# Kernel tuning notes

Measured on AMD Instinct MI355X. Metric: run time of the kernel, lower is better.

The kernel has to match this reference:

```python
import jax, jax.numpy as jnp
import numpy as np

WINDOW = 60
DEPTH = 3
HIDDEN = 256
LN_EPS = 1e-5


def _lyndon_indices(d):
    # Lyndon words over alphabet {0..d-1}, lengths 2 and 3, lexicographic order
    # (signatory mode='words' extracts expanded-logsig coefficients at Lyndon words).
    i2 = np.array([(i, j) for i in range(d) for j in range(d) if (i, j) < (j, i)], dtype=np.int32)
    i3 = np.array([(i, j, k) for i in range(d) for j in range(d) for k in range(d)
                   if (i, j, k) < (j, k, i) and (i, j, k) < (k, i, j)], dtype=np.int32)
    return i2, i3


def _logsig_features(x):
    # x: [b, s, c] -> logsignature of time-augmented sliding windows: [b*s, sig_channels]
    b, s, c = x.shape
    d = c + 1
    # replicate-padded sliding windows via clipped gather (matches F.pad replicate + unfold)
    pos = jnp.clip(jnp.arange(s)[:, None] + jnp.arange(WINDOW)[None, :] - (WINDOW - 1), 0, s - 1)
    windows = x[:, pos, :]                                   # [b, s, W, c]
    t = jnp.linspace(0.0, 1.0, WINDOW, dtype=x.dtype)        # time augmentation channel
    t_b = jnp.broadcast_to(t[None, None, :, None], (b, s, WINDOW, 1))
    aug = jnp.concatenate([t_b, windows], axis=-1).reshape(b * s, WINDOW, d)
    N = b * s
    # basepoint=True: prepend zero point -> increments include the first point itself
    inc = jnp.diff(aug, axis=1, prepend=jnp.zeros((N, 1, d), aug.dtype))  # [N, W, d]
    inc_t = jnp.transpose(inc, (1, 0, 2))                    # [W, N, d]

    def chen_step(carry, v):
        S1, S2, S3 = carry
        vv = jnp.einsum('ni,nj->nij', v, v)
        vvv = jnp.einsum('nij,nk->nijk', vv, v)
        nS3 = S3 + jnp.einsum('nij,nk->nijk', S2, v) \
                 + 0.5 * jnp.einsum('ni,njk->nijk', S1, vv) + vvv / 6.0
        nS2 = S2 + jnp.einsum('ni,nj->nij', S1, v) + 0.5 * vv
        nS1 = S1 + v
        return (nS1, nS2, nS3), None

    init = (jnp.zeros((N, d), x.dtype), jnp.zeros((N, d, d), x.dtype), jnp.zeros((N, d, d, d), x.dtype))
    (S1, S2, S3), _ = jax.lax.scan(chen_step, init, inc_t)
    # log in truncated tensor algebra: log(1+x) = x - x^2/2 + x^3/3
    L1 = S1
    L2 = S2 - 0.5 * jnp.einsum('ni,nj->nij', S1, S1)
    L3 = (S3 - 0.5 * (jnp.einsum('ni,njk->nijk', S1, S2) + jnp.einsum('nij,nk->nijk', S2, S1))
          + jnp.einsum('ni,nj,nk->nijk', S1, S1, S1) / 3.0)
    i2, i3 = _lyndon_indices(d)
    f2 = L2[:, i2[:, 0], i2[:, 1]]
    f3 = L3[:, i3[:, 0], i3[:, 1], i3[:, 2]]
    return jnp.concatenate([L1, f2, f3], axis=-1)            # [N, sig_channels]


def setup_inputs() -> dict:
    key = jax.random.key(0)
    ks = jax.random.split(key, 5)
    b, s, c = 8, 2048, 8
    d = c + 1
    sig_channels = d + (d * d - d) // 2 + (d ** 3 - d) // 3  # 285 for d=9
    h2 = 2 * HIDDEN
    x = jax.random.normal(ks[0], (b, s, c), dtype=jnp.float32)
    w1 = jax.random.normal(ks[1], (sig_channels, h2), dtype=jnp.float32) / np.sqrt(sig_channels)
    b1 = jnp.zeros((h2,), jnp.float32)
    ln_g = jnp.ones((h2,), jnp.float32)
    ln_b = jnp.zeros((h2,), jnp.float32)
    w2 = jax.random.normal(ks[2], (h2, HIDDEN), dtype=jnp.float32) / np.sqrt(h2)
    b2 = jnp.zeros((HIDDEN,), jnp.float32)
    return {"x": x, "w1": w1, "b1": b1, "ln_g": ln_g, "ln_b": ln_b, "w2": w2, "b2": b2}


def reference(x, w1, b1, ln_g, ln_b, w2, b2):
    b, s, _ = x.shape
    feats = _logsig_features(x)                              # [b*s, sig_channels]
    h = jax.nn.gelu(feats @ w1 + b1, approximate=False)      # torch default GELU (erf)
    mu = jnp.mean(h, axis=-1, keepdims=True)
    var = jnp.var(h, axis=-1, keepdims=True)
    h = (h - mu) / jnp.sqrt(var + LN_EPS) * ln_g + ln_b      # LayerNorm; Dropout is eval no-op
    out = h @ w2 + b2
    return out.reshape(b, s, -1)
```

## Files before the change

kernel.cpp:

```cpp
#include <hip/hip_runtime.h>
#include <hip/hip_bf16.h>
#include <cstdint>
#include <cstddef>

typedef short short8 __attribute__((ext_vector_type(8)));
typedef float f32x4 __attribute__((ext_vector_type(4)));
typedef float f32x2 __attribute__((ext_vector_type(2)));

#define NS    2048
#define KPAD  288
#define H2    512
#define HID   256
#define WPB   7
#define SBLK  293

#define MFMA(a,b,c) __builtin_amdgcn_mfma_f32_16x16x32_bf16((a),(b),(c),0,0,0)

__device__ __forceinline__ void gl2lds16(const void* g, void* l) {
    __builtin_amdgcn_global_load_lds(
        (const __attribute__((address_space(1))) void*)g,
        (__attribute__((address_space(3))) void*)l, 16, 0, 0);
}
__device__ __forceinline__ float geluf(float x) {
    return 0.5f * x * (1.0f + erff(x * 0.70710678118654752f));
}
__device__ __forceinline__ f32x4 shfl4(f32x4 v, int d) {
    f32x4 r;
    r[0] = __shfl_xor(v[0], d); r[1] = __shfl_xor(v[1], d);
    r[2] = __shfl_xor(v[2], d); r[3] = __shfl_xor(v[3], d);
    return r;
}

struct Tbl3 { short col[729]; };
static constexpr Tbl3 make_tbl3() {
    Tbl3 t{};
    for (int x = 0; x < 729; ++x) t.col[x] = -1;
    int r = 0;
    for (int i = 0; i < 9; ++i)
        for (int j = 0; j < 9; ++j)
            for (int k = 0; k < 9; ++k) {
                bool lt1 = (i < j) || (i == j && (j < k || (j == k && k < i)));
                bool lt2 = (i < k) || (i == k && (j < i || (j == i && k < j)));
                if (lt1 && lt2) { t.col[(i*9+j)*9+k] = (short)(45 + r); ++r; }
            }
    return t;
}
static constexpr Tbl3 TBL3 = make_tbl3();

#define SIG_STEP(VA_,VB_,VC_) { \
    const float hh = 0.5f * S1i + vi * (1.0f/6.0f); \
    const float ra = S2ra + hh * (VA_); \
    const float rb = S2rb + hh * (VB_); \
    const float rc = S2rc + hh * (VC_); \
    const f32x2 ra2 = {ra, ra}, rb2 = {rb, rb}, rc2 = {rc, rc}; \
    S3sa += ra * v0; S3pa0 += ra2*vp0; S3pa1 += ra2*vp1; S3pa2 += ra2*vp2; S3pa3 += ra2*vp3; \
    S3sb += rb * v0; S3pb0 += rb2*vp0; S3pb1 += rb2*vp1; S3pb2 += rb2*vp2; S3pb3 += rb2*vp3; \
    S3sc += rc * v0; S3pc0 += rc2*vp0; S3pc1 += rc2*vp1; S3pc2 += rc2*vp2; S3pc3 += rc2*vp3; \
    const float aa = S1i + 0.5f * vi; \
    S2ra += aa * (VA_); S2rb += aa * (VB_); S2rc += aa * (VC_); \
    S1i += vi; }

#define SIG_MAIN(VA_,VB_,VC_) { \
    { const float* xr = &X[(g0 - lo) * 8]; \
      const float4 e0 = *(const float4*)xr; \
      const float4 e1 = *(const float4*)(xr + 4); \
      const float rs = xr[ioff]; \
      const float v0 = 0.0f; \
      const f32x2 vp0 = {e0.x, e0.y}, vp1 = {e0.z, e0.w}, vp2 = {e1.x, e1.y}, vp3 = {e1.z, e1.w}; \
      const float vi = (ci == 0) ? 0.0f : rs; \
      SIG_STEP(VA_,VB_,VC_) } \
    const float* pd = &PD[(sm59 + 1 - lo + 59) * 8]; \
    float4 d0 = *(const float4*)pd; \
    float4 d1 = *(const float4*)(pd + 4); \
    float rn = pd[ioff]; \
    _Pragma("unroll 2") \
    for (int j = 1; j < 60; ++j) { \
      const float4 e0 = d0; const float4 e1 = d1; const float rs = rn; \
      pd += 8; \
      d0 = *(const float4*)pd; d1 = *(const float4*)(pd + 4); rn = pd[ioff]; \
      const float v0 = DT; \
      const f32x2 vp0 = {e0.x, e0.y}, vp1 = {e0.z, e0.w}, vp2 = {e1.x, e1.y}, vp3 = {e1.z, e1.w}; \
      const float vi = (ci == 0) ? DT : rs; \
      SIG_STEP(VA_,VB_,VC_) \
    } }

#define SIG_ST(RA,RB,RC) \
    if (act) { \
        if ((RA) == 0) S1buf[widx * 9 + ci] = S1i; \
        float* sb = &S2buf[widx * 81 + ci * 9]; \
        sb[RA] = S2ra; sb[RB] = S2rb; sb[RC] = S2rc; \
    }

#define S3EL0(SL) S3s##SL
#define S3EL1(SL) S3p##SL##0[0]
#define S3EL2(SL) S3p##SL##0[1]
#define S3EL3(SL) S3p##SL##1[0]
#define S3EL4(SL) S3p##SL##1[1]
#define S3EL5(SL) S3p##SL##2[0]
#define S3EL6(SL) S3p##SL##2[1]
#define S3EL7(SL) S3p##SL##3[0]
#define S3EL8(SL) S3p##SL##3[1]

#define SIG_E2(SL,J2) if (ci < (J2)) { \
    const float val2 = S2r##SL - 0.5f * S1i * s1v##J2; \
    const int col2 = 9 + ci*8 - (ci*(ci-1))/2 + ((J2) - ci - 1); \
    frow[col2] = __float2bfloat16(val2); }

#define SIG_E3(SL,R,K) { const int col3 = TBL3.col[tb + (R)*9 + (K)]; \
    if (col3 >= 0) { \
        const float val3 = S3EL##K(SL) \
            - 0.5f * (S1i * S2w[(R)*9+(K)] + S2r##SL * s1v##K) \
            + S1i * s1v##R * s1v##K * (1.0f/3.0f); \
        frow[col3] = __float2bfloat16(val3); } }

#define SIG_E3R(SL,R) SIG_E3(SL,R,0) SIG_E3(SL,R,1) SIG_E3(SL,R,2) SIG_E3(SL,R,3) \
    SIG_E3(SL,R,4) SIG_E3(SL,R,5) SIG_E3(SL,R,6) SIG_E3(SL,R,7) SIG_E3(SL,R,8)

#define SIG_EMIT(RA,RB,RC) \
    if (act) { \
        if ((RA) == 0) { \
            frow[ci] = __float2bfloat16(S1i); \
            if (ci == 0) { \
                const __hip_bfloat16 z16 = __float2bfloat16(0.0f); \
                frow[285] = z16; frow[286] = z16; frow[287] = z16; \
            } \
        } \
        SIG_E2(a,RA) SIG_E2(b,RB) SIG_E2(c,RC) \
        SIG_E3R(a,RA) SIG_E3R(b,RB) SIG_E3R(c,RC) \
    }

__global__ __launch_bounds__(192) __attribute__((amdgpu_waves_per_eu(1, 6)))
void sig_kernel(const float* __restrict__ x, __hip_bfloat16* __restrict__ feats) {
    __shared__ __align__(16) float X[66 * 8];
    __shared__ __align__(16) float PD[126 * 8];
    __shared__ float S2buf[WPB * 81];
    __shared__ float S1buf[WPB * 9];

    const int blk = blockIdx.x;
    const int b   = blk / SBLK;
    const int s0  = (blk % SBLK) * WPB;
    const int lo  = (s0 - 59 > 0) ? (s0 - 59) : 0;
    const int hi  = (s0 + WPB - 1 < NS - 1) ? (s0 + WPB - 1) : (NS - 1);
    const int nrow = hi - lo + 1;
    const int tid = threadIdx.x;

    {
        const float4* src = (const float4*)(x + ((size_t)b * NS + lo) * 8);
        float4* X4 = (float4*)X;
        const int n4 = nrow * 2;
        for (int t = tid; t < n4; t += 192) X4[t] = src[t];
    }
    __syncthreads();
    {
        const float4* X4 = (const float4*)X;
        float4* PD4 = (float4*)PD;
        for (int t = tid; t < 252; t += 192) {
            const int p = t >> 1;
            const int r = p - 59;
            float4 dv = {0.f, 0.f, 0.f, 0.f};
            if (r > 0 && r < nrow) {
                const float4 a = X4[t - 118], bb = X4[t - 120];
                dv.x = a.x - bb.x; dv.y = a.y - bb.y; dv.z = a.z - bb.z; dv.w = a.w - bb.w;
            }
            PD4[t] = dv;
        }
    }
    __syncthreads();

    const int t3    = tid >> 6;
    const int lt    = tid & 63;
    const int widx0 = lt / 9;
    const int ci    = lt - widx0 * 9;
    const bool act  = (lt < 63) && (s0 + widx0 < NS);
    const int widx  = (widx0 < WPB - 1) ? widx0 : WPB - 1;
    int s = s0 + widx; if (s > NS - 1) s = NS - 1;

    float S3sa=0.f, S3sb=0.f, S3sc=0.f;
    f32x2 S3pa0={0.f,0.f},S3pa1={0.f,0.f},S3pa2={0.f,0.f},S3pa3={0.f,0.f};
    f32x2 S3pb0={0.f,0.f},S3pb1={0.f,0.f},S3pb2={0.f,0.f},S3pb3={0.f,0.f};
    f32x2 S3pc0={0.f,0.f},S3pc1={0.f,0.f},S3pc2={0.f,0.f},S3pc3={0.f,0.f};
    float S2ra=0.f, S2rb=0.f, S2rc=0.f;
    float S1i = 0.f;
    const int ioff = (ci > 0) ? (ci - 1) : 0;
    const int sm59 = s - 59;
    const int g0   = (sm59 > 0) ? sm59 : 0;
    const float DT = 1.0f / 59.0f;

    if (t3 == 0)      { SIG_MAIN(v0,   e0.x, e0.y) }
    else if (t3 == 1) { SIG_MAIN(e0.z, e0.w, e1.x) }
    else              { SIG_MAIN(e1.y, e1.z, e1.w) }

    if (t3 == 0)      { SIG_ST(0,1,2) }
    else if (t3 == 1) { SIG_ST(3,4,5) }
    else              { SIG_ST(6,7,8) }
    __syncthreads();

    const float* s1p = &S1buf[widx * 9];
    const float s1v0=s1p[0], s1v1=s1p[1], s1v2=s1p[2], s1v3=s1p[3], s1v4=s1p[4];
    const float s1v5=s1p[5], s1v6=s1p[6], s1v7=s1p[7], s1v8=s1p[8];
    const float* S2w = &S2buf[widx * 81];
    const int tb = ci * 81;
    __hip_bfloat16* frow = feats + (size_t)(b * NS + s) * KPAD;

    if (t3 == 0)      { SIG_EMIT(0,1,2) }
    else if (t3 == 1) { SIG_EMIT(3,4,5) }
    else              { SIG_EMIT(6,7,8) }
}

__global__ void convert_w1(const float* __restrict__ w1, __hip_bfloat16* __restrict__ w1T) {
    const int n = blockIdx.x;
    const int k = threadIdx.x;
    const float v = (k < 285) ? w1[(size_t)k * H2 + n] : 0.0f;
    w1T[(size_t)n * KPAD + k] = __float2bfloat16(v);
}
__global__ void convert_w2g(const float* __restrict__ w2, const float* __restrict__ lng,
                            const float* __restrict__ lnb, const float* __restrict__ b2,
                            __hip_bfloat16* __restrict__ w2g, float* __restrict__ gw,
                            float* __restrict__ cvec) {
    const int n = blockIdx.x, k = threadIdx.x;
    const float wv = w2[(size_t)k * HID + n];
    const float a = lng[k] * wv;
    const float c = lnb[k] * wv;
    w2g[(size_t)n * H2 + k] = __float2bfloat16(a);
    float ra = a, rc = c;
#pragma unroll
    for (int d = 1; d < 64; d <<= 1) { ra += __shfl_xor(ra, d); rc += __shfl_xor(rc, d); }
    __shared__ float r1[8], r2[8];
    const int wv_ = k >> 6, ln = k & 63;
    if (ln == 0) { r1[wv_] = ra; r2[wv_] = rc; }
    __syncthreads();
    if (k == 0) {
        float sa = 0.f, sc = 0.f;
#pragma unroll
        for (int i = 0; i < 8; ++i) { sa += r1[i]; sc += r2[i]; }
        gw[n] = sa; cvec[n] = sc + b2[n];
    }
}

#define GDECL \
    f32x4 acc00={0,0,0,0},acc01={0,0,0,0},acc02={0,0,0,0},acc03={0,0,0,0}; \
    f32x4 acc10={0,0,0,0},acc11={0,0,0,0},acc12={0,0,0,0},acc13={0,0,0,0}; \
    f32x4 acc20={0,0,0,0},acc21={0,0,0,0},acc22={0,0,0,0},acc23={0,0,0,0}; \
    f32x4 acc30={0,0,0,0},acc31={0,0,0,0},acc32={0,0,0,0},acc33={0,0,0,0};

#define GMROW(mf) { const short8 av = *(const short8*)(abase + (mf)*512); \
    acc##mf##0 = MFMA(av, b0v, acc##mf##0); acc##mf##1 = MFMA(av, b1v, acc##mf##1); \
    acc##mf##2 = MFMA(av, b2v, acc##mf##2); acc##mf##3 = MFMA(av, b3v, acc##mf##3); }

#define GEMM_KLOOP(APTR, BPTR, KD, KSTEPS) \
    _Pragma("unroll 1") \
    for (int kt = 0; kt < (KSTEPS); ++kt) { \
        const int K0 = kt * 32; \
        { int c = tid; \
          gl2lds16((APTR) + (size_t)(m0 + (c>>2))*(KD) + K0 + (c&3)*8, (char*)ldsA + (c & ~63)*16); \
          gl2lds16((BPTR) + (size_t)(n0 + (c>>2))*(KD) + K0 + (c&3)*8, (char*)ldsB + (c & ~63)*16); \
          c = tid + 256; \
          gl2lds16((APTR) + (size_t)(m0 + (c>>2))*(KD) + K0 + (c&3)*8, (char*)ldsA + (c & ~63)*16); \
          gl2lds16((BPTR) + (size_t)(n0 + (c>>2))*(KD) + K0 + (c&3)*8, (char*)ldsB + (c & ~63)*16); } \
        __syncthreads(); \
        const __hip_bfloat16* abase = ldsA + (mh + l16)*32 + quad*8; \
        const __hip_bfloat16* bbase = ldsB + (nh + l16)*32 + quad*8; \
        const short8 b0v = *(const short8*)(bbase); \
        const short8 b1v = *(const short8*)(bbase + 512); \
        const short8 b2v = *(const short8*)(bbase + 1024); \
        const short8 b3v = *(const short8*)(bbase + 1536); \
        GMROW(0) GMROW(1) GMROW(2) GMROW(3) \
        __syncthreads(); \
    }

#define G1EP(mf,nf) { \
    const int colv = n0 + nh + (nf)*16 + l16; \
    const float bv = bias[colv]; \
    f32x4 e; \
    e[0] = geluf(acc##mf##nf[0] + bv); e[1] = geluf(acc##mf##nf[1] + bv); \
    e[2] = geluf(acc##mf##nf[2] + bv); e[3] = geluf(acc##mf##nf[3] + bv); \
    const int rrow = m0 + mh + (mf)*16 + quad*4; \
    h1[(size_t)(rrow+0)*H2 + colv] = __float2bfloat16(e[0]); \
    h1[(size_t)(rrow+1)*H2 + colv] = __float2bfloat16(e[1]); \
    h1[(size_t)(rrow+2)*H2 + colv] = __float2bfloat16(e[2]); \
    h1[(size_t)(rrow+3)*H2 + colv] = __float2bfloat16(e[3]); \
    sum##mf += e; sq##mf += e*e; }

#define G1RED(mf) { \
    f32x4 s = sum##mf, q = sq##mf; \
    s += shfl4(s,1); q += shfl4(q,1); s += shfl4(s,2); q += shfl4(q,2); \
    s += shfl4(s,4); q += shfl4(q,4); s += shfl4(s,8); q += shfl4(q,8); \
    if (l16 == 0) { const int rrow = m0 + mh + (mf)*16 + quad*4; \
        atomicAdd(&stats[2*(rrow+0)],   s[0]); atomicAdd(&stats[2*(rrow+0)+1], q[0]); \
        atomicAdd(&stats[2*(rrow+1)],   s[1]); atomicAdd(&stats[2*(rrow+1)+1], q[1]); \
        atomicAdd(&stats[2*(rrow+2)],   s[2]); atomicAdd(&stats[2*(rrow+2)+1], q[2]); \
        atomicAdd(&stats[2*(rrow+3)],   s[3]); atomicAdd(&stats[2*(rrow+3)+1], q[3]); } }

__global__ __launch_bounds__(256) __attribute__((amdgpu_waves_per_eu(1, 4)))
void gemm1_kernel(const __hip_bfloat16* __restrict__ feats,
                  const __hip_bfloat16* __restrict__ w1T,
                  const float* __restrict__ bias,
                  __hip_bfloat16* __restrict__ h1,
                  float* __restrict__ stats) {
    __shared__ __align__(16) __hip_bfloat16 ldsA[128 * 32];
    __shared__ __align__(16) __hip_bfloat16 ldsB[128 * 32];
    const int tid  = threadIdx.x;
    const int wave = tid >> 6;
    const int lane = tid & 63;
    const int quad = lane >> 4;
    const int l16  = lane & 15;
    const int mh   = (wave >> 1) * 64;
    const int nh   = (wave & 1) * 64;
    const int m0   = blockIdx.x * 128;
    const int n0   = blockIdx.y * 128;
    GDECL
    GEMM_KLOOP(feats, w1T, KPAD, 9)
    f32x4 sum0={0,0,0,0},sum1={0,0,0,0},sum2={0,0,0,0},sum3={0,0,0,0};
    f32x4 sq0={0,0,0,0},sq1={0,0,0,0},sq2={0,0,0,0},sq3={0,0,0,0};
    G1EP(0,0) G1EP(0,1) G1EP(0,2) G1EP(0,3)
    G1EP(1,0) G1EP(1,1) G1EP(1,2) G1EP(1,3)
    G1EP(2,0) G1EP(2,1) G1EP(2,2) G1EP(2,3)
    G1EP(3,0) G1EP(3,1) G1EP(3,2) G1EP(3,3)
    G1RED(0) G1RED(1) G1RED(2) G1RED(3)
}

#define STATR(r) { const float su = stats[2*(rrow+(r))]; const float qu = stats[2*(rrow+(r))+1]; \
    const float m_ = su * (1.0f/512.0f); const float v_ = qu * (1.0f/512.0f) - m_*m_; \
    muv[r] = m_; rsv[r] = rsqrtf(v_ + 1e-5f); }

#define G2C(mf,nf) { const int colv = n0 + nh + (nf)*16 + l16; \
    const float g_ = gw[colv], c_ = cvec[colv]; \
    out[(size_t)(rrow+0)*HID + colv] = rsv[0]*(acc##mf##nf[0] - muv[0]*g_) + c_; \
    out[(size_t)(rrow+1)*HID + colv] = rsv[1]*(acc##mf##nf[1] - muv[1]*g_) + c_; \
    out[(size_t)(rrow+2)*HID + colv] = rsv[2]*(acc##mf##nf[2] - muv[2]*g_) + c_; \
    out[(size_t)(rrow+3)*HID + colv] = rsv[3]*(acc##mf##nf[3] - muv[3]*g_) + c_; }

#define G2EP(mf) { const int rrow = m0 + mh + (mf)*16 + quad*4; \
    f32x4 muv, rsv; \
    STATR(0) STATR(1) STATR(2) STATR(3) \
    G2C(mf,0) G2C(mf,1) G2C(mf,2) G2C(mf,3) }

__global__ __launch_bounds__(256) __attribute__((amdgpu_waves_per_eu(1, 4)))
void gemm2_kernel(const __hip_bfloat16* __restrict__ h1,
                  const __hip_bfloat16* __restrict__ w2g,
                  const float* __restrict__ stats,
                  const float* __restrict__ gw,
                  const float* __restrict__ cvec,
                  float* __restrict__ out) {
    __shared__ __align__(16) __hip_bfloat16 ldsA[128 * 32];
    __shared__ __align__(16) __hip_bfloat16 ldsB[128 * 32];
    const int tid  = threadIdx.x;
    const int wave = tid >> 6;
    const int lane = tid & 63;
    const int quad = lane >> 4;
    const int l16  = lane & 15;
    const int mh   = (wave >> 1) * 64;
    const int nh   = (wave & 1) * 64;
    const int m0   = blockIdx.x * 128;
    const int n0   = blockIdx.y * 128;
    GDECL
    GEMM_KLOOP(h1, w2g, H2, 16)
    G2EP(0) G2EP(1) G2EP(2) G2EP(3)
}

extern "C" void kernel_launch(void* const* d_in, const int* in_sizes, int n_in,
                              void* d_out, int out_size, void* d_ws, size_t ws_size,
                              hipStream_t stream) {
    const float* x   = (const float*)d_in[0];
    const float* w1  = (const float*)d_in[1];
    const float* b1  = (const float*)d_in[2];
    const float* lng = (const float*)d_in[3];
    const float* lnb = (const float*)d_in[4];
    const float* w2  = (const float*)d_in[5];
    const float* b2  = (const float*)d_in[6];
    float* out = (float*)d_out;

    char* ws = (char*)d_ws;
    __hip_bfloat16* feats = (__hip_bfloat16*)(ws);
    __hip_bfloat16* h1    = (__hip_bfloat16*)(ws + 9437184);
    __hip_bfloat16* w1T   = (__hip_bfloat16*)(ws + 26214400);
    __hip_bfloat16* w2g   = (__hip_bfloat16*)(ws + 26509312);
    float*          gw    = (float*)(ws + 26771456);
    float*          cvec  = (float*)(ws + 26775552);
    float*          stats = (float*)(ws + 26779648);

    hipMemsetAsync(stats, 0, 16384 * 2 * sizeof(float), stream);
    convert_w1<<<dim3(512), dim3(288), 0, stream>>>(w1, w1T);
    convert_w2g<<<dim3(256), dim3(512), 0, stream>>>(w2, lng, lnb, b2, w2g, gw, cvec);
    sig_kernel<<<dim3(8 * SBLK), dim3(192), 0, stream>>>(x, feats);
    gemm1_kernel<<<dim3(128, 4), dim3(256), 0, stream>>>(feats, w1T, b1, h1, stats);
    gemm2_kernel<<<dim3(128, 2), dim3(256), 0, stream>>>(h1, w2g, stats, gw, cvec, out);
}
```

Measured before the change: 164.5 us.

## Double-buffer GEMM LDS tiles and merge prep kernels with stats memset

Both GEMM kernels now use two LDS buffers, so the async global-to-LDS load for the next K step is issued before the MFMAs on the current one, with a single barrier per step instead of two. The memset and the two weight-conversion kernels are folded into one prep kernel to cut launch count. The cost is doubled LDS per block, which may lower occupancy, and the prep kernel must zero all stats entries (512 blocks × 64 covers 32768 floats).

```diff
diff --git a/kernel.cpp b/kernel.cpp
--- a/kernel.cpp
+++ b/kernel.cpp
@@ -207,33 +207,41 @@
     else              { SIG_EMIT(6,7,8) }
 }
 
-__global__ void convert_w1(const float* __restrict__ w1, __hip_bfloat16* __restrict__ w1T) {
-    const int n = blockIdx.x;
-    const int k = threadIdx.x;
-    const float v = (k < 285) ? w1[(size_t)k * H2 + n] : 0.0f;
-    w1T[(size_t)n * KPAD + k] = __float2bfloat16(v);
-}
-__global__ void convert_w2g(const float* __restrict__ w2, const float* __restrict__ lng,
-                            const float* __restrict__ lnb, const float* __restrict__ b2,
-                            __hip_bfloat16* __restrict__ w2g, float* __restrict__ gw,
-                            float* __restrict__ cvec) {
-    const int n = blockIdx.x, k = threadIdx.x;
-    const float wv = w2[(size_t)k * HID + n];
-    const float a = lng[k] * wv;
-    const float c = lnb[k] * wv;
-    w2g[(size_t)n * H2 + k] = __float2bfloat16(a);
-    float ra = a, rc = c;
+__global__ __launch_bounds__(512)
+void prep_kernel(const float* __restrict__ w1, const float* __restrict__ w2,
+                 const float* __restrict__ lng, const float* __restrict__ lnb,
+                 const float* __restrict__ b2,
+                 __hip_bfloat16* __restrict__ w1T, __hip_bfloat16* __restrict__ w2g,
+                 float* __restrict__ gw, float* __restrict__ cvec,
+                 float* __restrict__ stats) {
+    const int blk = blockIdx.x;
+    if (blk < 256) {
+        const int n = blk, k = threadIdx.x;
+        const float wv = w2[(size_t)k * HID + n];
+        const float a = lng[k] * wv;
+        const float c = lnb[k] * wv;
+        w2g[(size_t)n * H2 + k] = __float2bfloat16(a);
+        float ra = a, rc = c;
 #pragma unroll
-    for (int d = 1; d < 64; d <<= 1) { ra += __shfl_xor(ra, d); rc += __shfl_xor(rc, d); }
-    __shared__ float r1[8], r2[8];
-    const int wv_ = k >> 6, ln = k & 63;
-    if (ln == 0) { r1[wv_] = ra; r2[wv_] = rc; }
-    __syncthreads();
-    if (k == 0) {
-        float sa = 0.f, sc = 0.f;
+        for (int d = 1; d < 64; d <<= 1) { ra += __shfl_xor(ra, d); rc += __shfl_xor(rc, d); }
+        __shared__ float r1[8], r2[8];
+        const int wv_ = k >> 6, ln = k & 63;
+        if (ln == 0) { r1[wv_] = ra; r2[wv_] = rc; }
+        __syncthreads();
+        if (k == 0) {
+            float sa = 0.f, sc = 0.f;
 #pragma unroll
-        for (int i = 0; i < 8; ++i) { sa += r1[i]; sc += r2[i]; }
-        gw[n] = sa; cvec[n] = sc + b2[n];
+            for (int i = 0; i < 8; ++i) { sa += r1[i]; sc += r2[i]; }
+            gw[n] = sa; cvec[n] = sc + b2[n];
+        }
+    } else {
+        const int n = blk - 256;
+        const int k = threadIdx.x;
+        if (k < KPAD) {
+            const float v = (k < 285) ? w1[(size_t)k * H2 + n] : 0.0f;
+            w1T[(size_t)n * KPAD + k] = __float2bfloat16(v);
+        }
+        if (k < 64) stats[n * 64 + k] = 0.0f;
     }
 }
 
@@ -247,25 +255,36 @@
     acc##mf##0 = MFMA(av, b0v, acc##mf##0); acc##mf##1 = MFMA(av, b1v, acc##mf##1); \
     acc##mf##2 = MFMA(av, b2v, acc##mf##2); acc##mf##3 = MFMA(av, b3v, acc##mf##3); }
 
-#define GEMM_KLOOP(APTR, BPTR, KD, KSTEPS) \
+#define GSTAGE(APTR, BPTR, KD, K0, LA, LB) { \
+    int c = tid; \
+    gl2lds16((APTR) + (size_t)(m0 + (c>>2))*(KD) + (K0) + (c&3)*8, (char*)(LA) + (c & ~63)*16); \
+    gl2lds16((BPTR) + (size_t)(n0 + (c>>2))*(KD) + (K0) + (c&3)*8, (char*)(LB) + (c & ~63)*16); \
+    c = tid + 256; \
+    gl2lds16((APTR) + (size_t)(m0 + (c>>2))*(KD) + (K0) + (c&3)*8, (char*)(LA) + (c & ~63)*16); \
+    gl2lds16((BPTR) + (size_t)(n0 + (c>>2))*(KD) + (K0) + (c&3)*8, (char*)(LB) + (c & ~63)*16); }
+
+#define GCOMP(LA, LB) { \
+    const __hip_bfloat16* abase = (LA) + (mh + l16)*32 + quad*8; \
+    const __hip_bfloat16* bbase = (LB) + (nh + l16)*32 + quad*8; \
+    const short8 b0v = *(const short8*)(bbase); \
+    const short8 b1v = *(const short8*)(bbase + 512); \
+    const short8 b2v = *(const short8*)(bbase + 1024); \
+    const short8 b3v = *(const short8*)(bbase + 1536); \
+    GMROW(0) GMROW(1) GMROW(2) GMROW(3) }
+
+#define GEMM_PIPE(APTR, BPTR, KD, KSTEPS) \
+    GSTAGE(APTR, BPTR, KD, 0, ldsA0, ldsB0) \
+    __syncthreads(); \
     _Pragma("unroll 1") \
-    for (int kt = 0; kt < (KSTEPS); ++kt) { \
-        const int K0 = kt * 32; \
-        { int c = tid; \
-          gl2lds16((APTR) + (size_t)(m0 + (c>>2))*(KD) + K0 + (c&3)*8, (char*)ldsA + (c & ~63)*16); \
-          gl2lds16((BPTR) + (size_t)(n0 + (c>>2))*(KD) + K0 + (c&3)*8, (char*)ldsB + (c & ~63)*16); \
-          c = tid + 256; \
-          gl2lds16((APTR) + (size_t)(m0 + (c>>2))*(KD) + K0 + (c&3)*8, (char*)ldsA + (c & ~63)*16); \
-          gl2lds16((BPTR) + (size_t)(n0 + (c>>2))*(KD) + K0 + (c&3)*8, (char*)ldsB + (c & ~63)*16); } \
+    for (int kt = 0; kt < (KSTEPS); kt += 2) { \
+        if (kt + 1 < (KSTEPS)) { GSTAGE(APTR, BPTR, KD, (kt+1)*32, ldsA1, ldsB1) } \
+        GCOMP(ldsA0, ldsB0) \
         __syncthreads(); \
-        const __hip_bfloat16* abase = ldsA + (mh + l16)*32 + quad*8; \
-        const __hip_bfloat16* bbase = ldsB + (nh + l16)*32 + quad*8; \
-        const short8 b0v = *(const short8*)(bbase); \
-        const short8 b1v = *(const short8*)(bbase + 512); \
-        const short8 b2v = *(const short8*)(bbase + 1024); \
-        const short8 b3v = *(const short8*)(bbase + 1536); \
-        GMROW(0) GMROW(1) GMROW(2) GMROW(3) \
-        __syncthreads(); \
+        if (kt + 1 < (KSTEPS)) { \
+            if (kt + 2 < (KSTEPS)) { GSTAGE(APTR, BPTR, KD, (kt+2)*32, ldsA0, ldsB0) } \
+            GCOMP(ldsA1, ldsB1) \
+            __syncthreads(); \
+        } \
     }
 
 #define G1EP(mf,nf) { \
@@ -297,8 +316,10 @@
                   const float* __restrict__ bias,
                   __hip_bfloat16* __restrict__ h1,
                   float* __restrict__ stats) {
-    __shared__ __align__(16) __hip_bfloat16 ldsA[128 * 32];
-    __shared__ __align__(16) __hip_bfloat16 ldsB[128 * 32];
+    __shared__ __align__(16) __hip_bfloat16 ldsA0[128 * 32];
+    __shared__ __align__(16) __hip_bfloat16 ldsB0[128 * 32];
+    __shared__ __align__(16) __hip_bfloat16 ldsA1[128 * 32];
+    __shared__ __align__(16) __hip_bfloat16 ldsB1[128 * 32];
     const int tid  = threadIdx.x;
     const int wave = tid >> 6;
     const int lane = tid & 63;
@@ -309,7 +330,7 @@
     const int m0   = blockIdx.x * 128;
     const int n0   = blockIdx.y * 128;
     GDECL
-    GEMM_KLOOP(feats, w1T, KPAD, 9)
+    GEMM_PIPE(feats, w1T, KPAD, 9)
     f32x4 sum0={0,0,0,0},sum1={0,0,0,0},sum2={0,0,0,0},sum3={0,0,0,0};
     f32x4 sq0={0,0,0,0},sq1={0,0,0,0},sq2={0,0,0,0},sq3={0,0,0,0};
     G1EP(0,0) G1EP(0,1) G1EP(0,2) G1EP(0,3)
@@ -342,8 +363,10 @@
                   const float* __restrict__ gw,
                   const float* __restrict__ cvec,
                   float* __restrict__ out) {
-    __shared__ __align__(16) __hip_bfloat16 ldsA[128 * 32];
-    __shared__ __align__(16) __hip_bfloat16 ldsB[128 * 32];
+    __shared__ __align__(16) __hip_bfloat16 ldsA0[128 * 32];
+    __shared__ __align__(16) __hip_bfloat16 ldsB0[128 * 32];
+    __shared__ __align__(16) __hip_bfloat16 ldsA1[128 * 32];
+    __shared__ __align__(16) __hip_bfloat16 ldsB1[128 * 32];
     const int tid  = threadIdx.x;
     const int wave = tid >> 6;
     const int lane = tid & 63;
@@ -354,7 +377,7 @@
     const int m0   = blockIdx.x * 128;
     const int n0   = blockIdx.y * 128;
     GDECL
-    GEMM_KLOOP(h1, w2g, H2, 16)
+    GEMM_PIPE(h1, w2g, H2, 16)
     G2EP(0) G2EP(1) G2EP(2) G2EP(3)
 }
 
@@ -379,9 +402,8 @@
     float*          cvec  = (float*)(ws + 26775552);
     float*          stats = (float*)(ws + 26779648);
 
-    hipMemsetAsync(stats, 0, 16384 * 2 * sizeof(float), stream);
-    convert_w1<<<dim3(512), dim3(288), 0, stream>>>(w1, w1T);
-    convert_w2g<<<dim3(256), dim3(512), 0, stream>>>(w2, lng, lnb, b2, w2g, gw, cvec);
+    prep_kernel<<<dim3(768), dim3(512), 0, stream>>>(w1, w2, lng, lnb, b2,
+                                                     w1T, w2g, gw, cvec, stats);
     sig_kernel<<<dim3(8 * SBLK), dim3(192), 0, stream>>>(x, feats);
     gemm1_kernel<<<dim3(128, 4), dim3(256), 0, stream>>>(feats, w1T, b1, h1, stats);
     gemm2_kernel<<<dim3(128, 2), dim3(256), 0, stream>>>(h1, w2g, stats, gw, cvec, out);
```

New measurement: 155.5 us. -5.5%, faster.
